# Kernel tuning notes

Hardware: AMD Instinct MI355X
Metric: run time of the kernel (lower is better)

## Reference

```python
import jax, jax.numpy as jnp
import numpy as np

B, S, D, H = 2, 2048, 1024, 16
DK = D // H  # 64


def _quantum(x, W1, b1, W2, b2):
    # Stand-in for QuantumNeuralLayer: classical->quantum->classical, d_k -> d_k.
    return jnp.tanh(x @ W1 + b1) @ W2 + b2


def setup_inputs() -> dict:
    key = jax.random.key(0)
    ks = jax.random.split(key, 16)
    s = 1.0 / np.sqrt(DK)
    inp = {
        "q": jax.random.normal(ks[0], (B, S, D), dtype=jnp.float32),
        "k": jax.random.normal(ks[1], (B, S, D), dtype=jnp.float32),
        "v": jax.random.normal(ks[2], (B, S, D), dtype=jnp.float32),
    }
    names = ["q", "k", "v"]
    for i, n in enumerate(names):
        inp[f"W{n}1"] = jax.random.normal(ks[3 + 4 * i], (DK, DK), dtype=jnp.float32) * s
        inp[f"b{n}1"] = jnp.zeros((DK,), dtype=jnp.float32)
        inp[f"W{n}2"] = jax.random.normal(ks[4 + 4 * i], (DK, DK), dtype=jnp.float32) * s
        inp[f"b{n}2"] = jnp.zeros((DK,), dtype=jnp.float32)
    inp["Wo"] = jax.random.normal(ks[15], (D, D), dtype=jnp.float32) * (1.0 / np.sqrt(D))
    inp["bo"] = jnp.zeros((D,), dtype=jnp.float32)
    return inp


def reference(q, k, v, Wq1, bq1, Wq2, bq2, Wk1, bk1, Wk2, bk2,
              Wv1, bv1, Wv2, bv2, Wo, bo):
    b, s, _ = q.shape
    # split heads: [B, S, H, DK]
    qh = q.reshape(b, s, H, DK)
    kh = k.reshape(b, s, H, DK)
    vh = v.reshape(b, s, H, DK)
    # quantum per-feature transform on last dim
    qh = _quantum(qh, Wq1, bq1, Wq2, bq2)
    kh = _quantum(kh, Wk1, bk1, Wk2, bk2)
    vh = _quantum(vh, Wv1, bv1, Wv2, bv2)
    scale = 1.0 / jnp.sqrt(jnp.asarray(DK, dtype=qh.dtype))
    # scores: [B, H, S, S]
    scores = jnp.einsum("bqhd,bkhd->bhqk", qh, kh) * scale
    attn = jax.nn.softmax(scores, axis=-1)
    # context: [B, H, S, DK] -> [B, S, D]
    ctx = jnp.einsum("bhqk,bkhd->bqhd", attn, vh).reshape(b, s, D)
    return ctx @ Wo + bo
```

## Files before the change

### kernel.cpp

```cpp
#include <hip/hip_runtime.h>

#define B_ 2
#define S_ 2048
#define D_ 1024
#define H_ 16
#define DK_ 64

typedef float f32x4 __attribute__((ext_vector_type(4)));
typedef float f32x16 __attribute__((ext_vector_type(16)));
typedef short bf16x8 __attribute__((ext_vector_type(8)));

static __device__ __forceinline__ unsigned short f2bf(float f) {
  unsigned u = __float_as_uint(f);
  unsigned r = (u + 0x7FFFu + ((u >> 16) & 1u)) >> 16;
  return (unsigned short)r;
}

static __device__ __forceinline__ unsigned cvtpk_bf16(float lo, float hi) {
  unsigned r;
  asm("v_cvt_pk_bf16_f32 %0, %1, %2" : "=v"(r) : "v"(lo), "v"(hi));
  return r;
}

static __device__ __forceinline__ void load16_lds(const void* g, void* lds) {
  __builtin_amdgcn_global_load_lds(
      (const __attribute__((address_space(1))) unsigned int*)g,
      (__attribute__((address_space(3))) unsigned int*)lds, 16, 0, 0);
}

static __device__ __forceinline__ bf16x8 make_pa8(const float* p, int hi) {
  unsigned x1 = cvtpk_bf16(p[0], p[1]);
  unsigned x2 = cvtpk_bf16(p[2], p[3]);
  unsigned y1 = cvtpk_bf16(p[4], p[5]);
  unsigned y2 = cvtpk_bf16(p[6], p[7]);
  asm("v_permlane32_swap_b32 %0, %1" : "+v"(x1), "+v"(y1));
  asm("v_permlane32_swap_b32 %0, %1" : "+v"(x2), "+v"(y2));
  union {
    unsigned u[4];
    bf16x8 v;
  } pa;
  pa.u[0] = x1;
  pa.u[1] = x2;
  pa.u[2] = y1;
  pa.u[3] = y2;
  (void)hi;
  return pa.v;
}

static __device__ __forceinline__ float tanh_fast(float x) {
  float xc = fminf(fmaxf(x, -9.0f), 9.0f);
  float e = exp2f(xc * 2.88539008177792681472f);
  return (e - 1.0f) / (e + 1.0f);
}

__global__ __launch_bounds__(256) void quantum_fused(
    const float* __restrict__ xq, const float* __restrict__ xk,
    const float* __restrict__ xv,
    const float* __restrict__ Wq1, const float* __restrict__ bq1,
    const float* __restrict__ Wq2, const float* __restrict__ bq2,
    const float* __restrict__ Wk1, const float* __restrict__ bk1,
    const float* __restrict__ Wk2, const float* __restrict__ bk2,
    const float* __restrict__ Wv1, const float* __restrict__ bv1,
    const float* __restrict__ Wv2, const float* __restrict__ bv2,
    const float* __restrict__ Wo, unsigned short* __restrict__ WoT,
    unsigned short* __restrict__ qhb, unsigned short* __restrict__ khb,
    unsigned short* __restrict__ vtb, float qscale) {
  __shared__ float tt[64][65];

  const int tid = threadIdx.x;

  if (blockIdx.z == 3) {
    if (blockIdx.y >= 16) return;
    const int k0 = blockIdx.x * 64, n0 = blockIdx.y * 64;
    const int r = tid >> 4, c4 = tid & 15;
#pragma unroll
    for (int i = 0; i < 4; ++i) {
      float4 v = *(const float4*)&Wo[(size_t)(k0 + r + 16 * i) * D_ + n0 + c4 * 4];
      tt[r + 16 * i][c4 * 4 + 0] = v.x;
      tt[r + 16 * i][c4 * 4 + 1] = v.y;
      tt[r + 16 * i][c4 * 4 + 2] = v.z;
      tt[r + 16 * i][c4 * 4 + 3] = v.w;
    }
    __syncthreads();
    const int n = tid >> 2, kc = tid & 3;
    union {
      unsigned short u[16];
      uint4 v[2];
    } pk;
#pragma unroll
    for (int j = 0; j < 16; ++j) pk.u[j] = f2bf(tt[kc * 16 + j][n]);
    unsigned short* op = WoT + (size_t)(n0 + n) * D_ + k0 + kc * 16;
    *(uint4*)op = pk.v[0];
    *(uint4*)(op + 8) = pk.v[1];
    return;
  }

  const int w = tid >> 6;
  const int l = tid & 63;
  const int lq = l & 31;
  const int hi = l >> 5;
  const int bh = blockIdx.y;
  const int b = bh >> 4, h = bh & 15;
  const int s0w = blockIdx.x * 128 + w * 32;

  const float* x;
  const float* W1;
  const float* b1;
  const float* W2;
  const float* b2;
  unsigned short* outp;
  float scale = 1.0f;
  int vmode = 0;
  if (blockIdx.z == 0) {
    x = xq; W1 = Wq1; b1 = bq1; W2 = Wq2; b2 = bq2; outp = qhb;
    scale = qscale;
  } else if (blockIdx.z == 1) {
    x = xk; W1 = Wk1; b1 = bk1; W2 = Wk2; b2 = bk2; outp = khb;
  } else {
    x = xv; W1 = Wv1; b1 = bv1; W2 = Wv2; b2 = bv2; outp = vtb;
    vmode = 1;
  }

  bf16x8 w1f[2][4];
#pragma unroll
  for (int ca = 0; ca < 2; ++ca)
#pragma unroll
    for (int kc = 0; kc < 4; ++kc) {
      const float* wp = W1 + (size_t)(kc * 16 + hi * 8) * 64 + ca * 32 + lq;
      union {
        unsigned u[4];
        bf16x8 v;
      } ww;
#pragma unroll
      for (int jj = 0; jj < 4; ++jj)
        ww.u[jj] = cvtpk_bf16(wp[(2 * jj) * 64], wp[(2 * jj + 1) * 64]);
      w1f[ca][kc] = ww.v;
    }

  const float* xrow = x + (((size_t)b * S_ + s0w + lq) * H_ + h) * DK_;
  bf16x8 xf[4];
#pragma unroll
  for (int kc = 0; kc < 4; ++kc) {
    float4 f0 = *(const float4*)(xrow + kc * 16 + hi * 8);
    float4 f1 = *(const float4*)(xrow + kc * 16 + hi * 8 + 4);
    union {
      unsigned u[4];
      bf16x8 v;
    } xx;
    xx.u[0] = cvtpk_bf16(f0.x, f0.y);
    xx.u[1] = cvtpk_bf16(f0.z, f0.w);
    xx.u[2] = cvtpk_bf16(f1.x, f1.y);
    xx.u[3] = cvtpk_bf16(f1.z, f1.w);
    xf[kc] = xx.v;
  }

  f32x16 acc1[2];
#pragma unroll
  for (int ca = 0; ca < 2; ++ca)
#pragma unroll
    for (int r = 0; r < 16; ++r)
      acc1[ca][r] = b1[ca * 32 + (r & 3) + 8 * (r >> 2) + 4 * hi];
#pragma unroll
  for (int kc = 0; kc < 4; ++kc) {
    acc1[0] = __builtin_amdgcn_mfma_f32_32x32x16_bf16(w1f[0][kc], xf[kc], acc1[0], 0, 0, 0);
    acc1[1] = __builtin_amdgcn_mfma_f32_32x32x16_bf16(w1f[1][kc], xf[kc], acc1[1], 0, 0, 0);
  }

  float t0[16], t1[16];
#pragma unroll
  for (int r = 0; r < 16; ++r) {
    t0[r] = tanh_fast(acc1[0][r]);
    t1[r] = tanh_fast(acc1[1][r]);
  }

  bf16x8 af[4];
  af[0] = make_pa8(&t0[0], hi);
  af[1] = make_pa8(&t0[8], hi);
  af[2] = make_pa8(&t1[0], hi);
  af[3] = make_pa8(&t1[8], hi);

  bf16x8 w2f[2][4];
#pragma unroll
  for (int nb = 0; nb < 2; ++nb)
#pragma unroll
    for (int kc = 0; kc < 4; ++kc) {
      const float* wp = W2 + (size_t)(kc * 16 + hi * 8) * 64 + nb * 32 + lq;
      union {
        unsigned u[4];
        bf16x8 v;
      } ww;
#pragma unroll
      for (int jj = 0; jj < 4; ++jj)
        ww.u[jj] = cvtpk_bf16(wp[(2 * jj) * 64], wp[(2 * jj + 1) * 64]);
      w2f[nb][kc] = ww.v;
    }

  f32x16 acc2[2];
#pragma unroll
  for (int nb = 0; nb < 2; ++nb)
#pragma unroll
    for (int r = 0; r < 16; ++r)
      acc2[nb][r] = b2[nb * 32 + (r & 3) + 8 * (r >> 2) + 4 * hi];
#pragma unroll
  for (int kc = 0; kc < 4; ++kc) {
    acc2[0] = __builtin_amdgcn_mfma_f32_32x32x16_bf16(af[kc], w2f[0][kc], acc2[0], 0, 0, 0);
    acc2[1] = __builtin_amdgcn_mfma_f32_32x32x16_bf16(af[kc], w2f[1][kc], acc2[1], 0, 0, 0);
  }

  if (!vmode) {
#pragma unroll
    for (int nb = 0; nb < 2; ++nb)
#pragma unroll
      for (int r = 0; r < 16; ++r) {
        const int s = s0w + (r & 3) + 8 * (r >> 2) + 4 * hi;
        outp[((size_t)bh * S_ + s) * DK_ + nb * 32 + lq] =
            f2bf(acc2[nb][r] * scale);
      }
  } else {
#pragma unroll
    for (int nb = 0; nb < 2; ++nb) {
      float yv[16];
#pragma unroll
      for (int r = 0; r < 16; ++r) yv[r] = acc2[nb][r];
      const size_t rowb = ((size_t)bh * DK_ + nb * 32 + lq) * S_;
      *(bf16x8*)(outp + rowb + s0w + hi * 8) = make_pa8(&yv[0], hi);
      *(bf16x8*)(outp + rowb + s0w + 16 + hi * 8) = make_pa8(&yv[8], hi);
    }
  }
}

__global__ __launch_bounds__(512, 4) void attn_kernel(
    const unsigned short* __restrict__ qhb,
    const unsigned short* __restrict__ khb,
    const unsigned short* __restrict__ vtb,
    unsigned short* __restrict__ ctxb) {
  __shared__ __align__(16) unsigned short kvbuf[2][2][64 * 64];
  __shared__ float mlseg[128];

  const int tid = threadIdx.x;
  const int w = tid >> 6;
  const int l = tid & 63;
  const int lq = l & 31;
  const int hi = l >> 5;
  const int qg = w & 3;
  const int khalf = w >> 2;
  const int bh = blockIdx.x;
  const int b = bh >> 4, h = bh & 15;
  const int q0 = blockIdx.y * 128 + qg * 32;

  const unsigned short* qp = qhb + ((size_t)bh * S_ + q0 + lq) * DK_ + hi * 8;
  bf16x8 qf[4];
#pragma unroll
  for (int kc = 0; kc < 4; ++kc) qf[kc] = *(const bf16x8*)(qp + kc * 16);

  f32x16 o0 = {}, o1 = {};
  f32x16 lacc = {};

  union {
    unsigned u[4];
    bf16x8 v;
  } onesu;
  onesu.u[0] = 0x3F803F80u;
  onesu.u[1] = 0x3F803F80u;
  onesu.u[2] = 0x3F803F80u;
  onesu.u[3] = 0x3F803F80u;
  const bf16x8 ones = onesu.v;

  const unsigned short* kgbase = khb + (size_t)bh * S_ * DK_;
  const unsigned short* vgbase = vtb + (size_t)bh * DK_ * S_;
  const int r0 = w * 8 + (l >> 3);
  const int sl8 = ((l & 7) ^ (l >> 3)) * 8;

  const unsigned short* kp = kgbase + (size_t)r0 * DK_ + sl8;
  const unsigned short* vp = vgbase + (size_t)r0 * S_ + sl8;

#define STAGE(BUF)                                                            \
  {                                                                           \
    load16_lds(kp, (char*)kvbuf[BUF][0] + w * 1024);                          \
    load16_lds(vp, (char*)kvbuf[BUF][1] + w * 1024);                          \
    kp += 64 * DK_;                                                           \
    vp += 64;                                                                 \
  }

  STAGE(0)
  __syncthreads();

  const int kr = khalf * 32 + lq;

  for (int t = 0; t < 32; ++t) {
    const int cur = t & 1;
    const char* ksP = (const char*)kvbuf[cur][0];
    const char* vsP = (const char*)kvbuf[cur][1];
    if (t < 31) STAGE(cur ^ 1)

    f32x16 s0 = {};
    __builtin_amdgcn_s_setprio(1);
#pragma unroll
    for (int kc = 0; kc < 4; ++kc) {
      bf16x8 k0 = *(const bf16x8*)(ksP + kr * 128 + (((kc * 2 + hi) ^ (kr & 7)) << 4));
      s0 = __builtin_amdgcn_mfma_f32_32x32x16_bf16(k0, qf[kc], s0, 0, 0, 0);
    }
    __builtin_amdgcn_s_setprio(0);

#pragma unroll
    for (int i = 0; i < 16; ++i) s0[i] = exp2f(s0[i]);

    float pv[8];
    __builtin_amdgcn_s_setprio(1);
#pragma unroll
    for (int kc = 0; kc < 2; ++kc) {
#pragma unroll
      for (int j = 0; j < 8; ++j) pv[j] = s0[kc * 8 + j];
      bf16x8 pav = make_pa8(pv, hi);
      const int slot = khalf * 4 + kc * 2 + hi;
      bf16x8 v0 = *(const bf16x8*)(vsP + lq * 128 + ((slot ^ (lq & 7)) << 4));
      bf16x8 v1 = *(const bf16x8*)(vsP + (32 + lq) * 128 + ((slot ^ (lq & 7)) << 4));
      o0 = __builtin_amdgcn_mfma_f32_32x32x16_bf16(pav, v0, o0, 0, 0, 0);
      o1 = __builtin_amdgcn_mfma_f32_32x32x16_bf16(pav, v1, o1, 0, 0, 0);
      lacc = __builtin_amdgcn_mfma_f32_32x32x16_bf16(pav, ones, lacc, 0, 0, 0);
    }
    __builtin_amdgcn_s_setprio(0);

    __syncthreads();
  }
#undef STAGE

  float* ksf = (float*)&kvbuf[0][0][0];
  const int qlb = qg * 32;

  if (khalf == 1) {
#pragma unroll
    for (int r = 0; r < 16; ++r) {
      const int ql = qlb + (r & 3) + 8 * (r >> 2) + 4 * hi;
      ksf[ql * 64 + lq] = o0[r];
      ksf[ql * 64 + 32 + lq] = o1[r];
      if (lq == 0) mlseg[ql] = lacc[r];
    }
  }
  __syncthreads();

  if (khalf == 0) {
#pragma unroll
    for (int r = 0; r < 16; ++r) {
      const int crow = ((r & 3) + 8 * (r >> 2)) + 4 * hi;
      const int ql = qlb + crow;
      const float li = 1.0f / (lacc[r] + mlseg[ql]);
      const int qg_ = blockIdx.y * 128 + ql;
      const size_t base = ((size_t)b * S_ + qg_) * D_ + h * DK_;
      ctxb[base + lq] = f2bf((o0[r] + ksf[ql * 64 + lq]) * li);
      ctxb[base + 32 + lq] = f2bf((o1[r] + ksf[ql * 64 + 32 + lq]) * li);
    }
  }
}

__global__ __launch_bounds__(256) void out_gemm_mfma(
    const unsigned short* __restrict__ A,
    const unsigned short* __restrict__ BT,
    const float* __restrict__ bo, float* __restrict__ C) {
  __shared__ __align__(16) unsigned short As[3][128 * 64];
  __shared__ __align__(16) unsigned short Bs[3][128 * 64];

  const int tid = threadIdx.x;
  const int w = tid >> 6, l = tid & 63;
  const int ll = l & 15, lg = l >> 4;
  const int wr = w >> 1, wc = w & 1;
  const int m0 = blockIdx.y * 128, n0 = blockIdx.x * 128;

  const int srow = l >> 3;
  const int sslot = (l & 7) ^ srow;
  const int g_off = sslot * 8;

  f32x4 acc[4][4];
#pragma unroll
  for (int mt = 0; mt < 4; ++mt)
#pragma unroll
    for (int nt = 0; nt < 4; ++nt) acc[mt][nt] = (f32x4){0.f, 0.f, 0.f, 0.f};

#define STAGE_G(BUF, KT)                                                      \
  {                                                                           \
    const int k0e = (KT)*64;                                                  \
    _Pragma("unroll") for (int c = 0; c < 4; ++c) {                           \
      const int row = c * 32 + w * 8 + srow;                                  \
      load16_lds(A + (size_t)(m0 + row) * D_ + k0e + g_off,                   \
                 (char*)As[BUF] + c * 4096 + w * 1024);                       \
      load16_lds(BT + (size_t)(n0 + row) * D_ + k0e + g_off,                  \
                 (char*)Bs[BUF] + c * 4096 + w * 1024);                       \
    }                                                                         \
  }

  STAGE_G(0, 0)
  STAGE_G(1, 1)

  for (int kt = 0; kt < 16; ++kt) {
    if (kt < 15) {
      asm volatile("s_waitcnt vmcnt(8)" ::: "memory");
    } else {
      asm volatile("s_waitcnt vmcnt(0)" ::: "memory");
    }
    __builtin_amdgcn_sched_barrier(0);
    __builtin_amdgcn_s_barrier();
    __builtin_amdgcn_sched_barrier(0);

    const int cur = kt % 3;
    if (kt < 14) STAGE_G((kt + 2) % 3, kt + 2)

#pragma unroll
    for (int half = 0; half < 2; ++half) {
      bf16x8 af[4], bfr[4];
#pragma unroll
      for (int mt = 0; mt < 4; ++mt) {
        const int row = wr * 64 + mt * 16 + ll;
        af[mt] = *(const bf16x8*)((const char*)As[cur] + row * 128 +
                                  (((half * 4 + lg) ^ (row & 7)) << 4));
      }
#pragma unroll
      for (int nt = 0; nt < 4; ++nt) {
        const int rowb = wc * 64 + nt * 16 + ll;
        bfr[nt] = *(const bf16x8*)((const char*)Bs[cur] + rowb * 128 +
                                   (((half * 4 + lg) ^ (rowb & 7)) << 4));
      }
      __builtin_amdgcn_s_setprio(1);
#pragma unroll
      for (int mt = 0; mt < 4; ++mt)
#pragma unroll
        for (int nt = 0; nt < 4; ++nt)
          acc[mt][nt] = __builtin_amdgcn_mfma_f32_16x16x32_bf16(
              af[mt], bfr[nt], acc[mt][nt], 0, 0, 0);
      __builtin_amdgcn_s_setprio(0);
    }
  }
#undef STAGE_G

#pragma unroll
  for (int nt = 0; nt < 4; ++nt) {
    const int col = n0 + wc * 64 + nt * 16 + ll;
    const float bv = bo[col];
#pragma unroll
    for (int mt = 0; mt < 4; ++mt) {
      const int row0 = m0 + wr * 64 + mt * 16 + lg * 4;
#pragma unroll
      for (int r = 0; r < 4; ++r)
        C[(size_t)(row0 + r) * D_ + col] = acc[mt][nt][r] + bv;
    }
  }
}

extern "C" void kernel_launch(void* const* d_in, const int* in_sizes, int n_in,
                              void* d_out, int out_size, void* d_ws,
                              size_t ws_size, hipStream_t stream) {
  const float* q = (const float*)d_in[0];
  const float* k = (const float*)d_in[1];
  const float* v = (const float*)d_in[2];
  const float* Wq1 = (const float*)d_in[3];
  const float* bq1 = (const float*)d_in[4];
  const float* Wq2 = (const float*)d_in[5];
  const float* bq2 = (const float*)d_in[6];
  const float* Wk1 = (const float*)d_in[7];
  const float* bk1 = (const float*)d_in[8];
  const float* Wk2 = (const float*)d_in[9];
  const float* bk2 = (const float*)d_in[10];
  const float* Wv1 = (const float*)d_in[11];
  const float* bv1 = (const float*)d_in[12];
  const float* Wv2 = (const float*)d_in[13];
  const float* bv2 = (const float*)d_in[14];
  const float* Wo = (const float*)d_in[15];
  const float* bo = (const float*)d_in[16];
  float* out = (float*)d_out;

  const size_t TEN = (size_t)B_ * H_ * S_ * DK_;
  char* ws = (char*)d_ws;
  unsigned short* qhb = (unsigned short*)ws;
  unsigned short* khb = (unsigned short*)(ws + TEN * 2);
  unsigned short* vtb = (unsigned short*)(ws + TEN * 4);
  unsigned short* ctxb = (unsigned short*)(ws + TEN * 6);
  unsigned short* wot = (unsigned short*)(ws + TEN * 8);

  const float cs = 0.125f * 1.44269504088896340736f;
  quantum_fused<<<dim3(16, 32, 4), 256, 0, stream>>>(
      q, k, v, Wq1, bq1, Wq2, bq2, Wk1, bk1, Wk2, bk2, Wv1, bv1, Wv2, bv2,
      Wo, wot, qhb, khb, vtb, cs);

  attn_kernel<<<dim3(32, 16), 512, 0, stream>>>(qhb, khb, vtb, ctxb);

  out_gemm_mfma<<<dim3(8, 32), 256, 0, stream>>>(ctxb, wot, bo, out);
}
```

Measured before the change: 102.3 us.

## Give each attention wave the full key tile and drop the split-K reduction

Each of the 8 waves now owns 32 query rows and processes all 64 keys per tile, so a block covers 256 queries instead of 128 and the grid halves. This removes the khalf split over keys and the LDS-based cross-wave reduction of partial outputs and row sums at the end. Each K/V tile loaded into LDS is now reused by twice as many queries. Per-wave work and register pressure double (two score accumulators), so launch bounds drop to 2 blocks per SM. The grid shrinks to 256 blocks, which may leave compute units underused.

```diff
diff --git a/kernel.cpp b/kernel.cpp
--- a/kernel.cpp
+++ b/kernel.cpp
@@ -229,24 +229,21 @@
   }
 }
 
-__global__ __launch_bounds__(512, 4) void attn_kernel(
+__global__ __launch_bounds__(512, 2) void attn_kernel(
     const unsigned short* __restrict__ qhb,
     const unsigned short* __restrict__ khb,
     const unsigned short* __restrict__ vtb,
     unsigned short* __restrict__ ctxb) {
   __shared__ __align__(16) unsigned short kvbuf[2][2][64 * 64];
-  __shared__ float mlseg[128];
 
   const int tid = threadIdx.x;
   const int w = tid >> 6;
   const int l = tid & 63;
   const int lq = l & 31;
   const int hi = l >> 5;
-  const int qg = w & 3;
-  const int khalf = w >> 2;
   const int bh = blockIdx.x;
   const int b = bh >> 4, h = bh & 15;
-  const int q0 = blockIdx.y * 128 + qg * 32;
+  const int q0 = blockIdx.y * 256 + w * 32;
 
   const unsigned short* qp = qhb + ((size_t)bh * S_ + q0 + lq) * DK_ + hi * 8;
   bf16x8 qf[4];
@@ -268,11 +265,11 @@
 
   const unsigned short* kgbase = khb + (size_t)bh * S_ * DK_;
   const unsigned short* vgbase = vtb + (size_t)bh * DK_ * S_;
-  const int r0 = w * 8 + (l >> 3);
-  const int sl8 = ((l & 7) ^ (l >> 3)) * 8;
-
-  const unsigned short* kp = kgbase + (size_t)r0 * DK_ + sl8;
-  const unsigned short* vp = vgbase + (size_t)r0 * S_ + sl8;
+  const int srow = tid >> 3;
+  const int sl8 = ((tid & 7) ^ (srow & 7)) * 8;
+
+  const unsigned short* kp = kgbase + (size_t)srow * DK_ + sl8;
+  const unsigned short* vp = vgbase + (size_t)srow * S_ + sl8;
 
 #define STAGE(BUF)                                                            \
   {                                                                           \
@@ -285,34 +282,38 @@
   STAGE(0)
   __syncthreads();
 
-  const int kr = khalf * 32 + lq;
-
   for (int t = 0; t < 32; ++t) {
     const int cur = t & 1;
     const char* ksP = (const char*)kvbuf[cur][0];
     const char* vsP = (const char*)kvbuf[cur][1];
     if (t < 31) STAGE(cur ^ 1)
 
-    f32x16 s0 = {};
+    f32x16 s0a = {}, s0b = {};
     __builtin_amdgcn_s_setprio(1);
 #pragma unroll
     for (int kc = 0; kc < 4; ++kc) {
-      bf16x8 k0 = *(const bf16x8*)(ksP + kr * 128 + (((kc * 2 + hi) ^ (kr & 7)) << 4));
-      s0 = __builtin_amdgcn_mfma_f32_32x32x16_bf16(k0, qf[kc], s0, 0, 0, 0);
+      const int so = ((kc * 2 + hi) ^ (lq & 7)) << 4;
+      bf16x8 ka = *(const bf16x8*)(ksP + lq * 128 + so);
+      bf16x8 kb = *(const bf16x8*)(ksP + (32 + lq) * 128 + so);
+      s0a = __builtin_amdgcn_mfma_f32_32x32x16_bf16(ka, qf[kc], s0a, 0, 0, 0);
+      s0b = __builtin_amdgcn_mfma_f32_32x32x16_bf16(kb, qf[kc], s0b, 0, 0, 0);
     }
     __builtin_amdgcn_s_setprio(0);
 
 #pragma unroll
-    for (int i = 0; i < 16; ++i) s0[i] = exp2f(s0[i]);
+    for (int i = 0; i < 16; ++i) s0a[i] = exp2f(s0a[i]);
+#pragma unroll
+    for (int i = 0; i < 16; ++i) s0b[i] = exp2f(s0b[i]);
 
     float pv[8];
     __builtin_amdgcn_s_setprio(1);
 #pragma unroll
-    for (int kc = 0; kc < 2; ++kc) {
-#pragma unroll
-      for (int j = 0; j < 8; ++j) pv[j] = s0[kc * 8 + j];
+    for (int kc = 0; kc < 4; ++kc) {
+#pragma unroll
+      for (int j = 0; j < 8; ++j) pv[j] = (kc < 2) ? s0a[(kc & 1) * 8 + j]
+                                                   : s0b[(kc & 1) * 8 + j];
       bf16x8 pav = make_pa8(pv, hi);
-      const int slot = khalf * 4 + kc * 2 + hi;
+      const int slot = kc * 2 + hi;
       bf16x8 v0 = *(const bf16x8*)(vsP + lq * 128 + ((slot ^ (lq & 7)) << 4));
       bf16x8 v1 = *(const bf16x8*)(vsP + (32 + lq) * 128 + ((slot ^ (lq & 7)) << 4));
       o0 = __builtin_amdgcn_mfma_f32_32x32x16_bf16(pav, v0, o0, 0, 0, 0);
@@ -325,31 +326,14 @@
   }
 #undef STAGE
 
-  float* ksf = (float*)&kvbuf[0][0][0];
-  const int qlb = qg * 32;
-
-  if (khalf == 1) {
-#pragma unroll
-    for (int r = 0; r < 16; ++r) {
-      const int ql = qlb + (r & 3) + 8 * (r >> 2) + 4 * hi;
-      ksf[ql * 64 + lq] = o0[r];
-      ksf[ql * 64 + 32 + lq] = o1[r];
-      if (lq == 0) mlseg[ql] = lacc[r];
-    }
-  }
-  __syncthreads();
-
-  if (khalf == 0) {
-#pragma unroll
-    for (int r = 0; r < 16; ++r) {
-      const int crow = ((r & 3) + 8 * (r >> 2)) + 4 * hi;
-      const int ql = qlb + crow;
-      const float li = 1.0f / (lacc[r] + mlseg[ql]);
-      const int qg_ = blockIdx.y * 128 + ql;
-      const size_t base = ((size_t)b * S_ + qg_) * D_ + h * DK_;
-      ctxb[base + lq] = f2bf((o0[r] + ksf[ql * 64 + lq]) * li);
-      ctxb[base + 32 + lq] = f2bf((o1[r] + ksf[ql * 64 + 32 + lq]) * li);
-    }
+#pragma unroll
+  for (int r = 0; r < 16; ++r) {
+    const int crow = ((r & 3) + 8 * (r >> 2)) + 4 * hi;
+    const float li = 1.0f / lacc[r];
+    const int qg = q0 + crow;
+    const size_t base = ((size_t)b * S_ + qg) * D_ + h * DK_;
+    ctxb[base + lq] = f2bf(o0[r] * li);
+    ctxb[base + 32 + lq] = f2bf(o1[r] * li);
   }
 }
 
@@ -480,7 +464,7 @@
       q, k, v, Wq1, bq1, Wq2, bq2, Wk1, bk1, Wk2, bk2, Wv1, bv1, Wv2, bv2,
       Wo, wot, qhb, khb, vtb, cs);
 
-  attn_kernel<<<dim3(32, 16), 512, 0, stream>>>(qhb, khb, vtb, ctxb);
+  attn_kernel<<<dim3(32, 8), 512, 0, stream>>>(qhb, khb, vtb, ctxb);
 
   out_gemm_mfma<<<dim3(8, 32), 256, 0, stream>>>(ctxb, wot, bo, out);
 }
```

After: 100.2 us. -2.1%, faster.
